# Performance work log

Measured on AMD Instinct MI355X. Metric: run time of the kernel, lower is better.

## Reference

```python
import jax, jax.numpy as jnp
import numpy as np
import math

HIDDEN_DIM = 1024
NUM_HEAD = 16
HEAD_DIM = HIDDEN_DIM // NUM_HEAD


def setup_inputs() -> dict:
    key = jax.random.key(0)
    ks = jax.random.split(key, 9)
    B, S, D = 2, 2048, HIDDEN_DIM
    scale = 1.0 / math.sqrt(D)
    x = jax.random.normal(ks[0], (B, S, D), dtype=jnp.float32)
    wq = jax.random.normal(ks[1], (D, D), dtype=jnp.float32) * scale
    bq = jnp.zeros((D,), dtype=jnp.float32)
    wk = jax.random.normal(ks[2], (D, D), dtype=jnp.float32) * scale
    bk = jnp.zeros((D,), dtype=jnp.float32)
    wv = jax.random.normal(ks[3], (D, D), dtype=jnp.float32) * scale
    bv = jnp.zeros((D,), dtype=jnp.float32)
    wo = jax.random.normal(ks[4], (D, D), dtype=jnp.float32) * scale
    bo = jnp.zeros((D,), dtype=jnp.float32)
    return {"x": x, "wq": wq, "bq": bq, "wk": wk, "bk": bk,
            "wv": wv, "bv": bv, "wo": wo, "bo": bo}


def reference(x, wq, bq, wk, bk, wv, bv, wo, bo):
    B, S, D = x.shape
    H, Hd = NUM_HEAD, HEAD_DIM
    # QKV projections (torch Linear: y = x @ W^T + b)
    q = (x @ wq.T + bq).reshape(B, S, H, Hd).transpose(0, 2, 1, 3)  # [B,H,S,Hd]
    k = (x @ wk.T + bk).reshape(B, S, H, Hd).transpose(0, 2, 1, 3)
    v = (x @ wv.T + bv).reshape(B, S, H, Hd).transpose(0, 2, 1, 3)
    logits = jnp.einsum('bhsd,bhtd->bhst', q, k) / jnp.sqrt(jnp.float32(Hd))
    scores = jax.nn.softmax(logits, axis=-1)  # [B,H,S,S]
    out = jnp.einsum('bhst,bhtd->bhsd', scores, v)
    out = out.transpose(0, 2, 1, 3).reshape(B, S, D)
    return out @ wo.T + bo
```

## Files before the change

kernel.cpp:

```cpp
#include <hip/hip_runtime.h>
#include <hip/hip_bf16.h>
#include <math.h>

#define DEV __device__ __forceinline__

typedef float f32x4 __attribute__((ext_vector_type(4)));
typedef float f32x16 __attribute__((ext_vector_type(16)));
typedef __bf16 b16x8 __attribute__((ext_vector_type(8)));
typedef unsigned short ushort_t;
typedef ushort_t u16x8 __attribute__((ext_vector_type(8)));

#define BATCH 2
#define SEQ 2048
#define DMODEL 1024
#define NHEAD 16
#define HDIM 64
#define MROWS (BATCH * SEQ)
#define LOG2E 1.44269504088896f

#define OFF_XB   ((size_t)0)
#define OFF_WB   ((size_t)4 * 1024 * 1024)
#define OFF_WOB  ((size_t)7 * 1024 * 1024)
#define OFF_QKV  ((size_t)8 * 1024 * 1024)
#define OFF_OB   ((size_t)20 * 1024 * 1024)

DEV ushort_t f2bf(float f) {
    union { float f; unsigned u; } v; v.f = f;
    unsigned r = v.u + 0x7fffu + ((v.u >> 16) & 1u);
    return (ushort_t)(r >> 16);
}

DEV unsigned cvt_pk_bf16(float lo, float hi) {
    unsigned r;
    asm("v_cvt_pk_bf16_f32 %0, %1, %2" : "=v"(r) : "v"(lo), "v"(hi));
    return r;
}

DEV void permswap(unsigned &a, unsigned &b) {
    asm("v_permlane32_swap_b32 %0, %1" : "+v"(a), "+v"(b));
}

DEV f32x4 mfma16(u16x8 a, u16x8 b, f32x4 c) {
    return __builtin_amdgcn_mfma_f32_16x16x32_bf16(
        __builtin_bit_cast(b16x8, a), __builtin_bit_cast(b16x8, b), c, 0, 0, 0);
}

DEV f32x16 mfma32(u16x8 a, u16x8 b, f32x16 c) {
    return __builtin_amdgcn_mfma_f32_32x32x16_bf16(
        __builtin_bit_cast(b16x8, a), __builtin_bit_cast(b16x8, b), c, 0, 0, 0);
}

DEV void gload_lds16(const ushort_t* g, ushort_t* l) {
    __builtin_amdgcn_global_load_lds(
        (const __attribute__((address_space(1))) unsigned int*)g,
        (__attribute__((address_space(3))) unsigned int*)l, 16, 0, 0);
}

__global__ __launch_bounds__(256) void convert5(
    const float* __restrict__ x, const float* __restrict__ wq,
    const float* __restrict__ wk, const float* __restrict__ wv,
    const float* __restrict__ wo,
    ushort_t* __restrict__ xb, ushort_t* __restrict__ wb, ushort_t* __restrict__ wob)
{
    const int ai = blockIdx.y;
    const float* src; ushort_t* dst; int n;
    if (ai == 0)      { src = x;  dst = xb;                 n = MROWS * DMODEL; }
    else if (ai == 1) { src = wq; dst = wb;                 n = DMODEL * DMODEL; }
    else if (ai == 2) { src = wk; dst = wb + 1024 * 1024;   n = DMODEL * DMODEL; }
    else if (ai == 3) { src = wv; dst = wb + 2 * 1024 * 1024; n = DMODEL * DMODEL; }
    else              { src = wo; dst = wob;                n = DMODEL * DMODEL; }
    int idx = (blockIdx.x * 256 + threadIdx.x) * 4;
    int stride = gridDim.x * 256 * 4;
    for (int i = idx; i < n; i += stride) {
        float4 f = *(const float4*)(src + i);
        ushort4 u;
        u.x = f2bf(f.x); u.y = f2bf(f.y); u.z = f2bf(f.z); u.w = f2bf(f.w);
        *(ushort4*)(dst + i) = u;
    }
}

#define SWZ(row, col) ((col) ^ (((row) & 7) << 3))
template<int MODE>
__global__ __launch_bounds__(256) void gemm_nt(
    const ushort_t* __restrict__ A,
    const ushort_t* __restrict__ W,
    const float* __restrict__ b0, const float* __restrict__ b1, const float* __restrict__ b2,
    ushort_t* __restrict__ obf,
    float* __restrict__ of32)
{
    __shared__ __attribute__((aligned(16))) ushort_t ldsA[128 * 64];
    __shared__ __attribute__((aligned(16))) ushort_t ldsB[64 * 64];

    const int t = threadIdx.x;
    const int l = blockIdx.x + 32 * blockIdx.y;
    const int xcd = l & 7, i0 = l >> 3;
    const int m0 = (4 * xcd + (i0 & 3)) * 128;
    const int n0 = (i0 >> 2) * 64;
    const int mat = blockIdx.z;
    const ushort_t* Wm = W + (size_t)mat * (1024 * 1024);
    const float* bias = (mat == 0) ? b0 : (mat == 1 ? b1 : b2);

    const int lane = t & 63, wave = t >> 6;
    const int wr = wave * 32;
    const int lr = lane & 15, lk = (lane >> 4) * 8;

    f32x4 acc[2][4] = {};

    for (int k0 = 0; k0 < DMODEL; k0 += 64) {
#pragma unroll
        for (int i = 0; i < 2; ++i) {
            int e = (i * 256 + t) * 8;
            int row = e >> 6, col = e & 63;
            gload_lds16(Wm + (size_t)(n0 + row) * DMODEL + k0 + SWZ(row, col), &ldsB[e]);
        }
#pragma unroll
        for (int i = 0; i < 4; ++i) {
            int e = (i * 256 + t) * 8;
            int row = e >> 6, col = e & 63;
            gload_lds16(A + (size_t)(m0 + row) * DMODEL + k0 + SWZ(row, col), &ldsA[e]);
        }
        __syncthreads();
#pragma unroll
        for (int kk = 0; kk < 2; ++kk) {
            u16x8 av[2], bv[4];
#pragma unroll
            for (int i = 0; i < 2; ++i) {
                int ar = wr + i * 16 + lr;
                av[i] = *(const u16x8*)&ldsA[ar * 64 + SWZ(ar, kk * 32 + lk)];
            }
#pragma unroll
            for (int i = 0; i < 4; ++i) {
                int br = i * 16 + lr;
                bv[i] = *(const u16x8*)&ldsB[br * 64 + SWZ(br, kk * 32 + lk)];
            }
            __builtin_amdgcn_s_setprio(1);
#pragma unroll
            for (int m = 0; m < 2; ++m)
#pragma unroll
                for (int n = 0; n < 4; ++n)
                    acc[m][n] = mfma16(av[m], bv[n], acc[m][n]);
            __builtin_amdgcn_s_setprio(0);
        }
        __syncthreads();
    }

    const int lgr = (lane >> 4) * 4;
    if (MODE == 0) {
        ushort_t* dst = obf + (size_t)mat * ((size_t)MROWS * DMODEL);
        if (mat < 2) {
            const float qscale = (mat == 0) ? (0.125f * LOG2E) : 1.0f;
#pragma unroll
            for (int m = 0; m < 2; ++m) {
                int row = m0 + wr + m * 16 + lgr;
#pragma unroll
                for (int n = 0; n < 4; ++n) {
                    int col = n0 + n * 16 + lr;
                    float bcol = bias[col];
                    int h = col >> 6, hd = col & 63;
#pragma unroll
                    for (int r = 0; r < 4; ++r) {
                        int rr = row + r;
                        int bb = rr >> 11, s = rr & 2047;
                        float v = (acc[m][n][r] + bcol) * qscale;
                        dst[(((size_t)bb * NHEAD + h) * SEQ + s) * HDIM + hd] = f2bf(v);
                    }
                }
            }
        } else {
#pragma unroll
            for (int m = 0; m < 2; ++m) {
                int row = m0 + wr + m * 16 + lgr;
                int bb = row >> 11, s = row & 2047;
#pragma unroll
                for (int n = 0; n < 4; ++n) {
                    int col = n0 + n * 16 + lr;
                    float bcol = bias[col];
                    int h = col >> 6, hd = col & 63;
                    ushort4 pk;
                    pk.x = f2bf(acc[m][n][0] + bcol);
                    pk.y = f2bf(acc[m][n][1] + bcol);
                    pk.z = f2bf(acc[m][n][2] + bcol);
                    pk.w = f2bf(acc[m][n][3] + bcol);
                    *(ushort4*)&dst[(((size_t)bb * NHEAD + h) * HDIM + hd) * SEQ + s] = pk;
                }
            }
        }
    } else {
#pragma unroll
        for (int m = 0; m < 2; ++m) {
            int row = m0 + wr + m * 16 + lgr;
#pragma unroll
            for (int n = 0; n < 4; ++n) {
                int col = n0 + n * 16 + lr;
                float bcol = b0[col];
#pragma unroll
                for (int r = 0; r < 4; ++r)
                    of32[(size_t)(row + r) * DMODEL + col] = acc[m][n][r] + bcol;
            }
        }
    }
}

__global__ __launch_bounds__(256, 2) void attn(
    const ushort_t* __restrict__ Q, const ushort_t* __restrict__ K,
    const ushort_t* __restrict__ Vt, ushort_t* __restrict__ O)
{
    __shared__ __attribute__((aligned(16))) ushort_t kt[128 * 72];
    __shared__ __attribute__((aligned(16))) ushort_t vt[64 * 136];

    const int t = threadIdx.x, lane = t & 63, wave = t >> 6;
    const int lq = lane & 31, hi = lane >> 5;

    const int id = blockIdx.x;
    const int swz = (id & 7) * 64 + (id >> 3);
    const int q0 = (swz & 15) * 128;
    const int h = (swz >> 4) & 15, b = swz >> 8;

    const size_t base = ((size_t)(b * NHEAD + h)) * (SEQ * HDIM);
    const ushort_t* Qh = Q + base;
    const ushort_t* Kh = K + base;
    const ushort_t* Vh = Vt + base;

    const int q0w = q0 + wave * 32;

    u16x8 qf[4];
#pragma unroll
    for (int step = 0; step < 4; ++step)
        qf[step] = *(const u16x8*)(Qh + (size_t)(q0w + lq) * HDIM + step * 16 + hi * 8);

    u16x8 onesf;
#pragma unroll
    for (int j = 0; j < 8; ++j) onesf[j] = 0x3F80;

    f32x16 o0 = {}, o1 = {};
    f32x16 lacc = {};

    const int krow = t >> 1, kc = (t & 1) * 32;
    const int vrow = t >> 2, vc = (t & 3) * 32;

    for (int t0 = 0; t0 < SEQ; t0 += 128) {
        {
            const ushort_t* kg = Kh + (size_t)(t0 + krow) * HDIM + kc;
            u16x8 ka = *(const u16x8*)kg;
            u16x8 kb = *(const u16x8*)(kg + 8);
            u16x8 kc2 = *(const u16x8*)(kg + 16);
            u16x8 kd = *(const u16x8*)(kg + 24);
            ushort_t* kl = &kt[krow * 72 + kc];
            *(u16x8*)(kl)      = ka;
            *(u16x8*)(kl + 8)  = kb;
            *(u16x8*)(kl + 16) = kc2;
            *(u16x8*)(kl + 24) = kd;
            const ushort_t* vg = Vh + (size_t)vrow * SEQ + t0 + vc;
            u16x8 va = *(const u16x8*)vg;
            u16x8 vb = *(const u16x8*)(vg + 8);
            u16x8 vc2 = *(const u16x8*)(vg + 16);
            u16x8 vd = *(const u16x8*)(vg + 24);
            ushort_t* vl = &vt[vrow * 136 + vc];
            *(u16x8*)(vl)      = va;
            *(u16x8*)(vl + 8)  = vb;
            *(u16x8*)(vl + 16) = vc2;
            *(u16x8*)(vl + 24) = vd;
        }
        __syncthreads();

        f32x16 sv[4] = {};
        __builtin_amdgcn_s_setprio(1);
#pragma unroll
        for (int step = 0; step < 4; ++step) {
#pragma unroll
            for (int n = 0; n < 4; ++n) {
                u16x8 kf = *(const u16x8*)&kt[(n * 32 + lq) * 72 + step * 16 + hi * 8];
                sv[n] = mfma32(kf, qf[step], sv[n]);
            }
        }
        __builtin_amdgcn_s_setprio(0);

#pragma unroll
        for (int n = 0; n < 4; ++n)
#pragma unroll
            for (int r = 0; r < 16; ++r)
                sv[n][r] = __builtin_amdgcn_exp2f(sv[n][r]);

        __builtin_amdgcn_s_setprio(1);
#pragma unroll
        for (int s = 0; s < 8; ++s) {
            const int n = s >> 1, g0 = (s & 1) * 2;
            unsigned xA = cvt_pk_bf16(sv[n][4 * g0 + 0], sv[n][4 * g0 + 1]);
            unsigned yA = cvt_pk_bf16(sv[n][4 * g0 + 2], sv[n][4 * g0 + 3]);
            unsigned xB = cvt_pk_bf16(sv[n][4 * g0 + 4], sv[n][4 * g0 + 5]);
            unsigned yB = cvt_pk_bf16(sv[n][4 * g0 + 6], sv[n][4 * g0 + 7]);
            permswap(xA, xB);
            permswap(yA, yB);
            uint4 w4; w4.x = xA; w4.y = yA; w4.z = xB; w4.w = yB;
            u16x8 pa = __builtin_bit_cast(u16x8, w4);
            u16x8 vf0 = *(const u16x8*)&vt[(lq)      * 136 + s * 16 + hi * 8];
            u16x8 vf1 = *(const u16x8*)&vt[(32 + lq) * 136 + s * 16 + hi * 8];
            o0 = mfma32(pa, vf0, o0);
            o1 = mfma32(pa, vf1, o1);
            lacc = mfma32(pa, onesf, lacc);
        }
        __builtin_amdgcn_s_setprio(0);
        __syncthreads();
    }

#pragma unroll
    for (int g = 0; g < 4; ++g) {
#pragma unroll
        for (int k = 0; k < 4; ++k) {
            int r = g * 4 + k;
            float linv = 1.0f / lacc[r];
            int sg = q0w + g * 8 + hi * 4 + k;
            size_t obase = ((size_t)(b * SEQ + sg)) * DMODEL + h * HDIM;
            O[obase + lq]      = f2bf(o0[r] * linv);
            O[obase + 32 + lq] = f2bf(o1[r] * linv);
        }
    }
}

extern "C" void kernel_launch(void* const* d_in, const int* in_sizes, int n_in,
                              void* d_out, int out_size, void* d_ws, size_t ws_size,
                              hipStream_t stream) {
    const float* x  = (const float*)d_in[0];
    const float* wq = (const float*)d_in[1];
    const float* bq = (const float*)d_in[2];
    const float* wk = (const float*)d_in[3];
    const float* bk = (const float*)d_in[4];
    const float* wv = (const float*)d_in[5];
    const float* bv = (const float*)d_in[6];
    const float* wo = (const float*)d_in[7];
    const float* bo = (const float*)d_in[8];
    float* out = (float*)d_out;

    ushort_t* ws  = (ushort_t*)d_ws;
    ushort_t* xb  = ws + OFF_XB;
    ushort_t* wb  = ws + OFF_WB;
    ushort_t* wob = ws + OFF_WOB;
    ushort_t* qkv = ws + OFF_QKV;
    ushort_t* Qb  = qkv;
    ushort_t* Kb  = qkv + (size_t)4 * 1024 * 1024;
    ushort_t* Vb  = qkv + (size_t)8 * 1024 * 1024;
    ushort_t* Ob  = ws + OFF_OB;

    convert5<<<dim3(1024, 5, 1), 256, 0, stream>>>(x, wq, wk, wv, wo, xb, wb, wob);
    gemm_nt<0><<<dim3(32, 16, 3), 256, 0, stream>>>(xb, wb, bq, bk, bv, qkv, nullptr);
    attn<<<dim3(512, 1, 1), 256, 0, stream>>>(Qb, Kb, Vb, Ob);
    gemm_nt<1><<<dim3(32, 16, 1), 256, 0, stream>>>(Ob, wob, bo, nullptr, nullptr, nullptr, out);
}
```

Measured before the change: 106.2 us.

## Split attention over two KV halves and merge with a combine kernel

Adds a templated split-KV path for the attention kernel. Each block handles half of the key sequence and writes unnormalized fp32 partial outputs and row sums to workspace. A new combine kernel adds the two halves, normalizes and writes bf16. The aim is to double the block count for better load balance across CUs, at the cost of extra fp32 global traffic and one more launch. The path is taken only when the workspace is large enough; otherwise the original kernel runs.

Result: slower. 118.5 us (+11.6%).

```diff
diff --git a/kernel.cpp b/kernel.cpp
--- a/kernel.cpp
+++ b/kernel.cpp
@@ -18,11 +18,14 @@
 #define MROWS (BATCH * SEQ)
 #define LOG2E 1.44269504088896f
 
-#define OFF_XB   ((size_t)0)
-#define OFF_WB   ((size_t)4 * 1024 * 1024)
-#define OFF_WOB  ((size_t)7 * 1024 * 1024)
-#define OFF_QKV  ((size_t)8 * 1024 * 1024)
-#define OFF_OB   ((size_t)20 * 1024 * 1024)
+#define OFF_XB    ((size_t)0)
+#define OFF_WB    ((size_t)4 * 1024 * 1024)
+#define OFF_WOB   ((size_t)7 * 1024 * 1024)
+#define OFF_QKV   ((size_t)8 * 1024 * 1024)
+#define OFF_OB    ((size_t)20 * 1024 * 1024)
+#define OFF_OPART ((size_t)24 * 1024 * 1024)
+#define OFF_LPART ((size_t)40 * 1024 * 1024)
+#define WS_NEED_BYTES ((size_t)42205184 * 2)
 
 DEV ushort_t f2bf(float f) {
     union { float f; unsigned u; } v; v.f = f;
@@ -201,9 +204,11 @@
     }
 }
 
+template<int SPLIT>
 __global__ __launch_bounds__(256, 2) void attn(
     const ushort_t* __restrict__ Q, const ushort_t* __restrict__ K,
-    const ushort_t* __restrict__ Vt, ushort_t* __restrict__ O)
+    const ushort_t* __restrict__ Vt, ushort_t* __restrict__ O,
+    float* __restrict__ opart, float* __restrict__ lpart)
 {
     __shared__ __attribute__((aligned(16))) ushort_t kt[128 * 72];
     __shared__ __attribute__((aligned(16))) ushort_t vt[64 * 136];
@@ -212,9 +217,17 @@
     const int lq = lane & 31, hi = lane >> 5;
 
     const int id = blockIdx.x;
-    const int swz = (id & 7) * 64 + (id >> 3);
-    const int q0 = (swz & 15) * 128;
-    const int h = (swz >> 4) & 15, b = swz >> 8;
+    int q0, h, b, sp, t_begin, t_end;
+    if (SPLIT == 0) {
+        const int swz = (id & 7) * 64 + (id >> 3);
+        q0 = (swz & 15) * 128; h = (swz >> 4) & 15; b = swz >> 8;
+        sp = 0; t_begin = 0; t_end = SEQ;
+    } else {
+        const int swz = (id & 7) * 128 + (id >> 3);
+        sp = swz & 1;
+        q0 = ((swz >> 1) & 15) * 128; h = (swz >> 5) & 15; b = swz >> 9;
+        t_begin = sp * (SEQ / 2); t_end = t_begin + SEQ / 2;
+    }
 
     const size_t base = ((size_t)(b * NHEAD + h)) * (SEQ * HDIM);
     const ushort_t* Qh = Q + base;
@@ -238,7 +251,7 @@
     const int krow = t >> 1, kc = (t & 1) * 32;
     const int vrow = t >> 2, vc = (t & 3) * 32;
 
-    for (int t0 = 0; t0 < SEQ; t0 += 128) {
+    for (int t0 = t_begin; t0 < t_end; t0 += 128) {
         {
             const ushort_t* kg = Kh + (size_t)(t0 + krow) * HDIM + kc;
             u16x8 ka = *(const u16x8*)kg;
@@ -303,18 +316,52 @@
         __syncthreads();
     }
 
-#pragma unroll
-    for (int g = 0; g < 4; ++g) {
-#pragma unroll
-        for (int k = 0; k < 4; ++k) {
-            int r = g * 4 + k;
-            float linv = 1.0f / lacc[r];
-            int sg = q0w + g * 8 + hi * 4 + k;
-            size_t obase = ((size_t)(b * SEQ + sg)) * DMODEL + h * HDIM;
-            O[obase + lq]      = f2bf(o0[r] * linv);
-            O[obase + 32 + lq] = f2bf(o1[r] * linv);
-        }
-    }
+    if (SPLIT == 0) {
+#pragma unroll
+        for (int g = 0; g < 4; ++g) {
+#pragma unroll
+            for (int k = 0; k < 4; ++k) {
+                int r = g * 4 + k;
+                float linv = 1.0f / lacc[r];
+                int sg = q0w + g * 8 + hi * 4 + k;
+                size_t obase = ((size_t)(b * SEQ + sg)) * DMODEL + h * HDIM;
+                O[obase + lq]      = f2bf(o0[r] * linv);
+                O[obase + 32 + lq] = f2bf(o1[r] * linv);
+            }
+        }
+    } else {
+#pragma unroll
+        for (int g = 0; g < 4; ++g) {
+#pragma unroll
+            for (int k = 0; k < 4; ++k) {
+                int r = g * 4 + k;
+                int sg = q0w + g * 8 + hi * 4 + k;
+                size_t rbase = (((size_t)(sp * 2 + b) * NHEAD + h) * SEQ + sg);
+                opart[rbase * 64 + lq]      = o0[r];
+                opart[rbase * 64 + 32 + lq] = o1[r];
+                if (lq == 0) lpart[rbase] = lacc[r];
+            }
+        }
+    }
+}
+
+__global__ __launch_bounds__(256) void attn_combine(
+    const float* __restrict__ opart, const float* __restrict__ lpart,
+    ushort_t* __restrict__ O)
+{
+    const int c = blockIdx.x * 256 + threadIdx.x;
+    const int dc = c & 15, s = (c >> 4) & 2047, h = (c >> 15) & 15, b = c >> 19;
+    const size_t r0 = (((size_t)(0 * 2 + b) * NHEAD + h) * SEQ + s);
+    const size_t r1 = (((size_t)(1 * 2 + b) * NHEAD + h) * SEQ + s);
+    float linv = 1.0f / (lpart[r0] + lpart[r1]);
+    float4 a = *(const float4*)&opart[r0 * 64 + dc * 4];
+    float4 d = *(const float4*)&opart[r1 * 64 + dc * 4];
+    ushort4 u;
+    u.x = f2bf((a.x + d.x) * linv);
+    u.y = f2bf((a.y + d.y) * linv);
+    u.z = f2bf((a.z + d.z) * linv);
+    u.w = f2bf((a.w + d.w) * linv);
+    *(ushort4*)&O[((size_t)(b * SEQ + s)) * DMODEL + h * HDIM + dc * 4] = u;
 }
 
 extern "C" void kernel_launch(void* const* d_in, const int* in_sizes, int n_in,
@@ -340,9 +387,16 @@
     ushort_t* Kb  = qkv + (size_t)4 * 1024 * 1024;
     ushort_t* Vb  = qkv + (size_t)8 * 1024 * 1024;
     ushort_t* Ob  = ws + OFF_OB;
+    float* opart  = (float*)(ws + OFF_OPART);
+    float* lpart  = (float*)(ws + OFF_LPART);
 
     convert5<<<dim3(1024, 5, 1), 256, 0, stream>>>(x, wq, wk, wv, wo, xb, wb, wob);
     gemm_nt<0><<<dim3(32, 16, 3), 256, 0, stream>>>(xb, wb, bq, bk, bv, qkv, nullptr);
-    attn<<<dim3(512, 1, 1), 256, 0, stream>>>(Qb, Kb, Vb, Ob);
+    if (ws_size >= WS_NEED_BYTES) {
+        attn<1><<<dim3(1024, 1, 1), 256, 0, stream>>>(Qb, Kb, Vb, nullptr, opart, lpart);
+        attn_combine<<<dim3(4096, 1, 1), 256, 0, stream>>>(opart, lpart, Ob);
+    } else {
+        attn<0><<<dim3(512, 1, 1), 256, 0, stream>>>(Qb, Kb, Vb, Ob, nullptr, nullptr);
+    }
     gemm_nt<1><<<dim3(32, 16, 1), 256, 0, stream>>>(Ob, wob, bo, nullptr, nullptr, nullptr, out);
 }
```
